# Performance work log

Measured on AMD Instinct MI355X. Metric: run time of the kernel, lower is better.

## Reference

```python
import jax, jax.numpy as jnp
import numpy as np

B, L, D, H, NL, DFF = 32, 64, 256, 8, 2, 2048
S, I, DSEM, DDENSE, DSPARSE = 16, 16, 128, 128, 128


def layer_norm(x, g, b, eps=1e-5):
    m = x.mean(-1, keepdims=True)
    v = ((x - m) ** 2).mean(-1, keepdims=True)
    return (x - m) / jnp.sqrt(v + eps) * g + b


def encoder_layer(x, ipw, ipb, ow, ob, g1, b1, g2, b2, f1w, f1b, f2w, f2b):
    # PyTorch TransformerEncoderLayer (post-norm, ReLU FFN, dropout inactive).
    b, t, d = x.shape
    dh = d // H
    qkv = x @ ipw.T + ipb  # (b,t,3d)
    q, k, v = jnp.split(qkv, 3, axis=-1)
    split_heads = lambda z: z.reshape(b, t, H, dh).transpose(0, 2, 1, 3)
    q, k, v = split_heads(q), split_heads(k), split_heads(v)
    att = jax.nn.softmax(jnp.einsum('bhqd,bhkd->bhqk', q, k) / np.float32(np.sqrt(dh)), axis=-1)
    o = jnp.einsum('bhqk,bhkd->bhqd', att, v).transpose(0, 2, 1, 3).reshape(b, t, d)
    x = layer_norm(x + o @ ow.T + ob, g1, b1)
    h = jax.nn.relu(x @ f1w.T + f1b) @ f2w.T + f2b
    return layer_norm(x + h, g2, b2)


def setup_inputs() -> dict:
    key = jax.random.key(0)
    ks = jax.random.split(key, 16)
    sc = np.float32(0.02)
    return dict(
        dense=jax.random.normal(ks[0], (B, L, DDENSE), jnp.float32),
        sparse=jax.random.normal(ks[1], (B, L, DSPARSE), jnp.float32),
        W_feat=jax.random.normal(ks[2], (DDENSE + DSPARSE, D), jnp.float32) * sc,
        b_feat=jnp.zeros((D,), jnp.float32),
        in_proj_w=jax.random.normal(ks[3], (NL, 3 * D, D), jnp.float32) * sc,
        in_proj_b=jnp.zeros((NL, 3 * D), jnp.float32),
        out_w=jax.random.normal(ks[4], (NL, D, D), jnp.float32) * sc,
        out_b=jnp.zeros((NL, D), jnp.float32),
        ln1_g=jnp.ones((NL, D), jnp.float32), ln1_b=jnp.zeros((NL, D), jnp.float32),
        ln2_g=jnp.ones((NL, D), jnp.float32), ln2_b=jnp.zeros((NL, D), jnp.float32),
        ff1_w=jax.random.normal(ks[5], (NL, DFF, D), jnp.float32) * sc,
        ff1_b=jnp.zeros((NL, DFF), jnp.float32),
        ff2_w=jax.random.normal(ks[6], (NL, D, DFF), jnp.float32) * sc,
        ff2_b=jnp.zeros((NL, D), jnp.float32),
        w_act=jax.random.normal(ks[7], (D, 1), jnp.float32) * sc,
        w_route_ws=jax.random.normal(ks[8], (L, S, D), jnp.float32) * sc,
        w_pose_ws=jax.random.normal(ks[9], (L, S, D, D), jnp.float32) * sc,
        w_route_si=jax.random.normal(ks[10], (S, I, D), jnp.float32) * sc,
        w_pose_si=jax.random.normal(ks[11], (S, I, D, D), jnp.float32) * sc,
        cls_w=jax.random.normal(ks[12], (DSEM, 2 * D), jnp.float32) * sc,
        cls_b=jnp.zeros((DSEM,), jnp.float32),
        inorm_g=jnp.ones((DSEM,), jnp.float32),
        inorm_b=jnp.zeros((DSEM,), jnp.float32),
    )


def reference(dense, sparse, W_feat, b_feat, in_proj_w, in_proj_b, out_w, out_b,
              ln1_g, ln1_b, ln2_g, ln2_b, ff1_w, ff1_b, ff2_w, ff2_b,
              w_act, w_route_ws, w_pose_ws, w_route_si, w_pose_si,
              cls_w, cls_b, inorm_g, inorm_b):
    # TokenFeaturizer: concat(dense, sparse) -> Linear -> (b,L,d)
    tok = jnp.concatenate([dense, sparse], axis=-1) @ W_feat + b_feat
    cls = tok.sum(axis=1, keepdims=True)  # einsum 'bld->bd' CLS token
    x = jnp.concatenate([tok, cls], axis=1)  # (b, L+1, d)
    for i in range(in_proj_w.shape[0]):
        x = encoder_layer(x, in_proj_w[i], in_proj_b[i], out_w[i], out_b[i],
                          ln1_g[i], ln1_b[i], ln2_g[i], ln2_b[i],
                          ff1_w[i], ff1_b[i], ff2_w[i], ff2_b[i])
    words, cls_tok = x[:, :L], x[:, L]  # (b,L,d), (b,d)

    # --- route words -> slots ('weighted_sig') ---
    a_words = jax.nn.sigmoid((words @ w_act)[..., 0])  # (b,L)
    c_ws = jax.nn.softmax(jnp.einsum('lsd,bld->bls', w_route_ws, words), axis=-1)
    a_num = jnp.einsum('bls,bl->bs', c_ws, a_words)
    a_slots = a_num / a_words.sum(axis=1, keepdims=True)
    u_hat = jnp.einsum('lsij,blj->blsi', w_pose_ws, words)  # (b,L,S,d)
    u_num = jnp.einsum('bls,bl,blsi->bsi', c_ws, a_words, u_hat)
    u_slots = u_num / a_num[..., None]  # (b,S,d)

    # --- route slots -> intents ---
    c_si = jax.nn.softmax(jnp.einsum('sid,bsd->bsi', w_route_si, u_slots), axis=-1)
    an = jnp.einsum('bsi,bs->bi', c_si, a_slots)
    a_intents = an / (a_slots.sum(axis=1, keepdims=True) + 1e-8)
    u_hat_i = jnp.einsum('sijk,bsk->bsik', w_pose_si, u_slots)  # (b,S,I,d)
    un = jnp.einsum('bsi,bs,bsik->bik', c_si, a_slots, u_hat_i)
    u_intents = un / (an[..., None] + 1e-8)  # (b,I,d)

    # argmax over intents, gather winning pose
    idx = jnp.argmax(a_intents, axis=-1)  # (b,)
    poses = u_intents[jnp.arange(u_intents.shape[0]), idx]  # (b,d)
    intents = jnp.concatenate([cls_tok, poses], axis=-1) @ cls_w.T + cls_b
    intents = layer_norm(intents, inorm_g, inorm_b)
    return (c_ws, intents)
```

## Files before the change

kernel.cpp:

```cpp
#include <hip/hip_runtime.h>
#include <hip/hip_bf16.h>
#include <math.h>

#define B_ 32
#define L_ 64
#define D_ 256
#define H_ 8
#define T_ 65
#define NT_ (B_*T_)
#define DFF_ 2048
#define S_ 16
#define I_ 16
#define DSEM_ 128

typedef __attribute__((ext_vector_type(8))) short bf16x8;
typedef __attribute__((ext_vector_type(4))) float f32x4;

typedef __attribute__((address_space(1))) const void gbl_void;
typedef __attribute__((address_space(3))) void lds_void;
#define GLOAD16(g, l) __builtin_amdgcn_global_load_lds((gbl_void*)(g), (lds_void*)(l), 16, 0, 0)

__device__ inline unsigned short f2bu(float f) {
  union { float f; unsigned u; } a; a.f = f;
  unsigned r = a.u + 0x7FFF + ((a.u >> 16) & 1);
  return (unsigned short)(r >> 16);
}
__device__ inline float b2f(unsigned short u) {
  union { unsigned u; float f; } a; a.u = ((unsigned)u) << 16;
  return a.f;
}

__device__ inline float wave_reduce_sum(float v) {
#pragma unroll
  for (int m = 32; m >= 1; m >>= 1) v += __shfl_xor(v, m, 64);
  return v;
}

__device__ inline float block_reduce_sum_256(float v, float* sred) {
  v = wave_reduce_sum(v);
  int tid = threadIdx.x;
  if ((tid & 63) == 0) sred[tid >> 6] = v;
  __syncthreads();
  float r = sred[0] + sred[1] + sred[2] + sred[3];
  __syncthreads();
  return r;
}

__global__ void concat_bf_kernel(const float* __restrict__ dense, const float* __restrict__ sparse,
                                 unsigned short* __restrict__ cat) {
  int idx = blockIdx.x * 256 + threadIdx.x;
  int r = idx >> 8, c = idx & 255;
  float v = (c < 128) ? dense[r * 128 + c] : sparse[r * 128 + (c - 128)];
  cat[idx] = f2bu(v);
}

__global__ void f2b4_kernel(const float* __restrict__ in, unsigned short* __restrict__ out, int n4) {
  int i = blockIdx.x * 256 + threadIdx.x;
  if (i < n4) {
    float4 v = ((const float4*)in)[i];
    short4 o;
    o.x = (short)f2bu(v.x); o.y = (short)f2bu(v.y);
    o.z = (short)f2bu(v.z); o.w = (short)f2bu(v.w);
    ((short4*)out)[i] = o;
  }
}

__global__ void transpose_f2b_kernel(const float* __restrict__ in, unsigned short* __restrict__ out) {
  int n = blockIdx.x, k = threadIdx.x;
  out[n * 256 + k] = f2bu(in[k * 256 + n]);
}

template <int ACT, int OUT_BF16, int NFRAG>
__global__ __launch_bounds__(256) void gemm_bf2_kernel(const unsigned short* __restrict__ A,
                                                       const unsigned short* __restrict__ W,
                                                       const float* __restrict__ bias,
                                                       float* __restrict__ Cf, unsigned short* __restrict__ Cb,
                                                       int M, int N, int K) {
  __shared__ __align__(16) unsigned short As[2][32 * 64];
  __shared__ __align__(16) unsigned short Bs[2][NFRAG * 64 * 64];
  int tid = threadIdx.x, wid = tid >> 6, lane = tid & 63;
  int row0 = blockIdx.y * 32, col0 = blockIdx.x * (64 * NFRAG);
  int lr = lane >> 3;
  int sc = ((lane & 7) ^ (lr & 7)) << 3;
  const unsigned short* Asrc = A + (size_t)(row0 + wid * 8 + lr) * K + sc;
  const unsigned short* Bsrc[2 * NFRAG];
#pragma unroll
  for (int p = 0; p < 2 * NFRAG; ++p)
    Bsrc[p] = W + (size_t)(col0 + wid * 16 * NFRAG + p * 8 + lr) * K + sc;
  unsigned short* AsW = &As[0][0] + wid * (8 * 64);
  unsigned short* BsW = &Bs[0][0] + wid * (16 * NFRAG * 64);

  f32x4 acc[2][NFRAG];
#pragma unroll
  for (int i = 0; i < 2; ++i)
#pragma unroll
    for (int j = 0; j < NFRAG; ++j) acc[i][j] = (f32x4){0.f, 0.f, 0.f, 0.f};

  GLOAD16(Asrc, AsW);
#pragma unroll
  for (int p = 0; p < 2 * NFRAG; ++p) GLOAD16(Bsrc[p], BsW + p * (8 * 64));

  int nk = K >> 6, cur = 0;
  int kg = lane >> 4, l15 = lane & 15;
  for (int kt = 0; kt < nk; ++kt) {
    __syncthreads();
    if (kt + 1 < nk) {
      int k0 = (kt + 1) << 6;
      GLOAD16(Asrc + k0, AsW + (cur ^ 1) * (32 * 64));
#pragma unroll
      for (int p = 0; p < 2 * NFRAG; ++p)
        GLOAD16(Bsrc[p] + k0, BsW + (cur ^ 1) * (NFRAG * 64 * 64) + p * (8 * 64));
    }
    const unsigned short* Ab = &As[cur][0];
    const unsigned short* Bb = &Bs[cur][0];
#pragma unroll
    for (int kk = 0; kk < 2; ++kk) {
      int cc = kk * 4 + kg;
      bf16x8 bfr[NFRAG];
#pragma unroll
      for (int fn = 0; fn < NFRAG; ++fn) {
        int rn = wid * 16 * NFRAG + fn * 16 + l15;
        bfr[fn] = *(const bf16x8*)&Bb[rn * 64 + ((cc ^ (rn & 7)) << 3)];
      }
#pragma unroll
      for (int fm = 0; fm < 2; ++fm) {
        int rm = fm * 16 + l15;
        bf16x8 afr = *(const bf16x8*)&Ab[rm * 64 + ((cc ^ (rm & 7)) << 3)];
#pragma unroll
        for (int fn = 0; fn < NFRAG; ++fn)
          acc[fm][fn] = __builtin_amdgcn_mfma_f32_16x16x32_bf16(afr, bfr[fn], acc[fm][fn], 0, 0, 0);
      }
    }
    cur ^= 1;
  }
#pragma unroll
  for (int fm = 0; fm < 2; ++fm) {
#pragma unroll
    for (int fn = 0; fn < NFRAG; ++fn) {
      int col = col0 + wid * 16 * NFRAG + fn * 16 + l15;
      float bi = bias[col];
      int rbase = row0 + fm * 16 + ((lane >> 4) << 2);
#pragma unroll
      for (int r = 0; r < 4; ++r) {
        int grow = rbase + r;
        float v = acc[fm][fn][r] + bi;
        if (ACT == 1) v = fmaxf(v, 0.f);
        if (OUT_BF16) Cb[(size_t)grow * N + col] = f2bu(v);
        else          Cf[(size_t)grow * N + col] = v;
      }
    }
  }
}

__global__ void build_x_kernel(const float* __restrict__ tok, float* __restrict__ x,
                               unsigned short* __restrict__ xbf) {
  int b = blockIdx.x, d = threadIdx.x;
  float s = 0.f;
  for (int l = 0; l < L_; ++l) {
    float v = tok[((size_t)(b * L_ + l)) * D_ + d];
    size_t o = ((size_t)(b * T_ + l)) * D_ + d;
    x[o] = v; xbf[o] = f2bu(v);
    s += v;
  }
  size_t o = ((size_t)(b * T_ + L_)) * D_ + d;
  x[o] = s; xbf[o] = f2bu(s);
}

__global__ __launch_bounds__(256) void attn_kernel(const unsigned short* __restrict__ qkv,
                                                   unsigned short* __restrict__ attn_out) {
  int bh = blockIdx.x;
  int b = bh >> 3, h = bh & 7;
  __shared__ float Q[T_][32], K[T_][32], V[T_][32];
  __shared__ float Sc[T_][T_ + 1];
  int tid = threadIdx.x;
  for (int idx = tid; idx < T_ * 32; idx += 256) {
    int t = idx >> 5, d = idx & 31;
    const unsigned short* base = qkv + ((size_t)(b * T_ + t)) * 768 + h * 32 + d;
    Q[t][d] = b2f(base[0]);
    K[t][d] = b2f(base[256]);
    V[t][d] = b2f(base[512]);
  }
  __syncthreads();
  for (int idx = tid; idx < T_ * T_; idx += 256) {
    int qi = idx / T_, ki = idx % T_;
    float s = 0.f;
#pragma unroll
    for (int d = 0; d < 32; ++d) s += Q[qi][d] * K[ki][d];
    Sc[qi][ki] = s * 0.17677669529663687f;
  }
  __syncthreads();
  if (tid < T_) {
    float mx = -1e30f;
    for (int k = 0; k < T_; ++k) mx = fmaxf(mx, Sc[tid][k]);
    float sum = 0.f;
    for (int k = 0; k < T_; ++k) { float e = expf(Sc[tid][k] - mx); Sc[tid][k] = e; sum += e; }
    float inv = 1.f / sum;
    for (int k = 0; k < T_; ++k) Sc[tid][k] *= inv;
  }
  __syncthreads();
  for (int idx = tid; idx < T_ * 32; idx += 256) {
    int t = idx >> 5, d = idx & 31;
    float acc = 0.f;
    for (int k = 0; k < T_; ++k) acc += Sc[t][k] * V[k][d];
    attn_out[((size_t)(b * T_ + t)) * D_ + h * 32 + d] = f2bu(acc);
  }
}

__global__ __launch_bounds__(256) void ln_residual_kernel(float* __restrict__ x, unsigned short* __restrict__ xbf,
                                                          const float* __restrict__ proj,
                                                          const float* __restrict__ g, const float* __restrict__ bb) {
  __shared__ float sred[4];
  int r = blockIdx.x, d = threadIdx.x;
  float v = x[(size_t)r * D_ + d] + proj[(size_t)r * D_ + d];
  float mean = block_reduce_sum_256(v, sred) * (1.f / 256.f);
  float dv = v - mean;
  float var = block_reduce_sum_256(dv * dv, sred) * (1.f / 256.f);
  float o = dv * (1.f / sqrtf(var + 1e-5f)) * g[d] + bb[d];
  x[(size_t)r * D_ + d] = o;
  xbf[(size_t)r * D_ + d] = f2bu(o);
}

__global__ __launch_bounds__(256) void cws_kernel(const float* __restrict__ x, const float* __restrict__ w_route,
                                                  const float* __restrict__ w_act, float* __restrict__ c_ws_out,
                                                  float* __restrict__ a_words) {
  int bl = blockIdx.x;
  int b = bl >> 6, l = bl & 63;
  __shared__ float word[256];
  __shared__ float logits[16];
  __shared__ float sred[4];
  int t = threadIdx.x;
  word[t] = x[((size_t)(b * T_ + l)) * D_ + t];
  __syncthreads();
  float pa = word[t] * w_act[t];
  float asum = block_reduce_sum_256(pa, sred);
  if (t == 0) a_words[b * 64 + l] = 1.f / (1.f + expf(-asum));
  int s = t >> 4, j0 = t & 15;
  float p = 0.f;
  for (int j = j0; j < 256; j += 16) p += w_route[((size_t)(l * 16 + s)) * 256 + j] * word[j];
#pragma unroll
  for (int m = 8; m >= 1; m >>= 1) p += __shfl_xor(p, m, 64);
  if (j0 == 0) logits[s] = p;
  __syncthreads();
  if (t < 16) {
    float mx = -1e30f;
#pragma unroll
    for (int k = 0; k < 16; ++k) mx = fmaxf(mx, logits[k]);
    float sum = 0.f;
#pragma unroll
    for (int k = 0; k < 16; ++k) sum += expf(logits[k] - mx);
    c_ws_out[(size_t)bl * 16 + t] = expf(logits[t] - mx) / sum;
  }
}

__global__ __launch_bounds__(64) void slot_agg_kernel(const float* __restrict__ c_ws, const float* __restrict__ a_words,
                                                      float* __restrict__ a_num, float* __restrict__ a_slots,
                                                      float* __restrict__ asl_sum) {
  int b = blockIdx.x, lane = threadIdx.x;
  float aw = a_words[b * 64 + lane];
  float asum = wave_reduce_sum(aw);
  float inv = 1.f / asum;
  float ssum = 0.f;
  for (int s = 0; s < 16; ++s) {
    float p = c_ws[((size_t)(b * 64 + lane)) * 16 + s] * aw;
    float r = wave_reduce_sum(p);
    if (lane == 0) {
      a_num[b * 16 + s] = r;
      a_slots[b * 16 + s] = r * inv;
      ssum += r * inv;
    }
  }
  if (lane == 0) asl_sum[b] = ssum;
}

__global__ __launch_bounds__(256, 4) void pose_ws2_kernel(const unsigned short* __restrict__ xbf,
                                                          const float* __restrict__ P,
                                                          const float* __restrict__ c_ws,
                                                          const float* __restrict__ a_words,
                                                          float* __restrict__ partial) {
  int lg = blockIdx.x >> 4, s = blockIdx.x & 15;
  __shared__ __align__(16) unsigned short Bs[32 * 256];
  int tid = threadIdx.x, wid = tid >> 6, lane = tid & 63;
  int kg = lane >> 4;
  f32x4 acc[4][2];
#pragma unroll
  for (int i = 0; i < 4; ++i)
#pragma unroll
    for (int j = 0; j < 2; ++j) acc[i][j] = (f32x4){0.f, 0.f, 0.f, 0.f};

#pragma unroll
  for (int li = 0; li < 2; ++li) {
    int l = lg + li * 32;
    __syncthreads();
    {
      int b = tid >> 3, c0 = (tid & 7) * 4;
      float w = c_ws[((size_t)(b * 64 + l)) * 16 + s] * a_words[b * 64 + l];
      const unsigned short* src = xbf + ((size_t)(b * T_ + l)) * D_;
#pragma unroll
      for (int j = 0; j < 4; ++j) {
        int c = c0 + j;
        union { float4 f4; unsigned short u[8]; } in, out;
        in.f4 = *(const float4*)(src + c * 8);
#pragma unroll
        for (int e = 0; e < 8; ++e) out.u[e] = f2bu(w * b2f(in.u[e]));
        *(float4*)&Bs[b * 256 + ((c ^ (b & 7)) << 3)] = out.f4;
      }
    }
    __syncthreads();
    const float* Pbase = P + (((size_t)(l * 16 + s)) << 16);
#pragma unroll
    for (int k0 = 0; k0 < 256; k0 += 64) {
#pragma unroll
      for (int kk = 0; kk < 2; ++kk) {
        int cc = (k0 >> 3) + kk * 4 + kg;
        bf16x8 bfr[2];
#pragma unroll
        for (int fn = 0; fn < 2; ++fn) {
          int rb = fn * 16 + (lane & 15);
          bfr[fn] = *(const bf16x8*)&Bs[rb * 256 + ((cc ^ (rb & 7)) << 3)];
        }
        int kbase = k0 + kk * 32 + kg * 8;
#pragma unroll
        for (int fm = 0; fm < 4; ++fm) {
          int row = wid * 64 + fm * 16 + (lane & 15);
          const float* src = Pbase + (size_t)row * 256 + kbase;
          float4 v0 = *(const float4*)src;
          float4 v1 = *(const float4*)(src + 4);
          union { bf16x8 b8; unsigned short u[8]; } pk;
          pk.u[0] = f2bu(v0.x); pk.u[1] = f2bu(v0.y); pk.u[2] = f2bu(v0.z); pk.u[3] = f2bu(v0.w);
          pk.u[4] = f2bu(v1.x); pk.u[5] = f2bu(v1.y); pk.u[6] = f2bu(v1.z); pk.u[7] = f2bu(v1.w);
          acc[fm][0] = __builtin_amdgcn_mfma_f32_16x16x32_bf16(pk.b8, bfr[0], acc[fm][0], 0, 0, 0);
          acc[fm][1] = __builtin_amdgcn_mfma_f32_16x16x32_bf16(pk.b8, bfr[1], acc[fm][1], 0, 0, 0);
        }
      }
    }
  }
  float* pout = partial + ((size_t)(lg * 16 + s)) * 8192;
#pragma unroll
  for (int fm = 0; fm < 4; ++fm) {
#pragma unroll
    for (int fn = 0; fn < 2; ++fn) {
      int b = fn * 16 + (lane & 15);
      int i0 = wid * 64 + fm * 16 + ((lane >> 4) << 2);
#pragma unroll
      for (int r = 0; r < 4; ++r)
        pout[(i0 + r) * 32 + b] = acc[fm][fn][r];
    }
  }
}

__global__ __launch_bounds__(256) void reduce_uslots_kernel(const float* __restrict__ partial,
                                                            const float* __restrict__ a_num,
                                                            float* __restrict__ u_slots) {
  int s = blockIdx.x >> 5, ic = blockIdx.x & 31;
  int t = threadIdx.x;
  int i = ic * 8 + (t >> 5), b = t & 31;
  size_t off = (size_t)s * 8192 + i * 32 + b;
  float a0 = 0.f, a1 = 0.f, a2 = 0.f, a3 = 0.f;
#pragma unroll
  for (int lg = 0; lg < 32; lg += 4) {
    a0 += partial[((size_t)(lg + 0) * 16) * 8192 + off];
    a1 += partial[((size_t)(lg + 1) * 16) * 8192 + off];
    a2 += partial[((size_t)(lg + 2) * 16) * 8192 + off];
    a3 += partial[((size_t)(lg + 3) * 16) * 8192 + off];
  }
  u_slots[((size_t)(b * 16 + s)) * 256 + i] = (a0 + a1 + a2 + a3) / a_num[b * 16 + s];
}

__global__ __launch_bounds__(256) void csi_kernel(const float* __restrict__ u_slots, const float* __restrict__ w_route_si,
                                                  float* __restrict__ c_si) {
  int bs = blockIdx.x;
  int s = bs & 15;
  __shared__ float row[256];
  __shared__ float logits[16];
  int t = threadIdx.x;
  row[t] = u_slots[(size_t)bs * 256 + t];
  __syncthreads();
  int i = t >> 4, j0 = t & 15;
  float p = 0.f;
  for (int j = j0; j < 256; j += 16) p += w_route_si[((size_t)(s * 16 + i)) * 256 + j] * row[j];
#pragma unroll
  for (int m = 8; m >= 1; m >>= 1) p += __shfl_xor(p, m, 64);
  if (j0 == 0) logits[i] = p;
  __syncthreads();
  if (t < 16) {
    float mx = -1e30f;
#pragma unroll
    for (int k = 0; k < 16; ++k) mx = fmaxf(mx, logits[k]);
    float sum = 0.f;
#pragma unroll
    for (int k = 0; k < 16; ++k) sum += expf(logits[k] - mx);
    c_si[(size_t)bs * 16 + t] = expf(logits[t] - mx) / sum;
  }
}

__global__ __launch_bounds__(64) void intent_agg_kernel(const float* __restrict__ c_si, const float* __restrict__ a_slots,
                                                        const float* __restrict__ asl_sum, float* __restrict__ an,
                                                        int* __restrict__ idxb) {
  int b = blockIdx.x, lane = threadIdx.x;
  __shared__ float an_s[16];
  if (lane < 16) {
    float acc = 0.f;
    for (int s = 0; s < 16; ++s) acc += c_si[((size_t)(b * 16 + s)) * 16 + lane] * a_slots[b * 16 + s];
    an[b * 16 + lane] = acc;
    an_s[lane] = acc;
  }
  __syncthreads();
  if (lane == 0) {
    float inv = 1.f / (asl_sum[b] + 1e-8f);
    int best = 0;
    float bv = an_s[0] * inv;
    for (int k = 1; k < 16; ++k) {
      float v = an_s[k] * inv;
      if (v > bv) { bv = v; best = k; }
    }
    idxb[b] = best;
  }
}

__global__ void pose_si_partial_kernel(const float* __restrict__ P, float* __restrict__ R4) {
  int si = blockIdx.x >> 2, jc = blockIdx.x & 3;
  int k = threadIdx.x;
  const float* base = P + (size_t)si * 65536 + (size_t)jc * 64 * 256 + k;
  float a0 = 0.f, a1 = 0.f, a2 = 0.f, a3 = 0.f;
#pragma unroll
  for (int j = 0; j < 64; j += 4) {
    a0 += base[(j + 0) * 256];
    a1 += base[(j + 1) * 256];
    a2 += base[(j + 2) * 256];
    a3 += base[(j + 3) * 256];
  }
  R4[(size_t)jc * 65536 + si * 256 + k] = a0 + a1 + a2 + a3;
}

__global__ void r4sum_kernel(const float* __restrict__ R4, float* __restrict__ R) {
  int idx = blockIdx.x * 256 + threadIdx.x;
  R[idx] = R4[idx] + R4[65536 + idx] + R4[131072 + idx] + R4[196608 + idx];
}

__global__ void un_kernel(const float* __restrict__ c_si, const float* __restrict__ a_slots,
                          const float* __restrict__ R, const float* __restrict__ u_slots,
                          const float* __restrict__ an, float* __restrict__ u_int) {
  int b = blockIdx.x >> 4, i = blockIdx.x & 15, k = threadIdx.x;
  float acc = 0.f;
  for (int s = 0; s < 16; ++s) {
    float w = c_si[((size_t)(b * 16 + s)) * 16 + i] * a_slots[b * 16 + s];
    acc += w * R[((size_t)(s * 16 + i)) * 256 + k] * u_slots[((size_t)(b * 16 + s)) * 256 + k];
  }
  u_int[((size_t)(b * 16 + i)) * 256 + k] = acc / (an[b * 16 + i] + 1e-8f);
}

__global__ __launch_bounds__(128) void final_kernel(const float* __restrict__ x, const float* __restrict__ u_int,
                                                    const int* __restrict__ idxb, const float* __restrict__ cls_w,
                                                    const float* __restrict__ cls_b, const float* __restrict__ g,
                                                    const float* __restrict__ bb, float* __restrict__ out) {
  int b = blockIdx.x, m = threadIdx.x;
  __shared__ float row[512];
  __shared__ float sred[2];
  int id = idxb[b];
  for (int d = m; d < 256; d += 128) {
    row[d] = x[((size_t)(b * T_ + L_)) * D_ + d];
    row[256 + d] = u_int[((size_t)(b * 16 + id)) * 256 + d];
  }
  __syncthreads();
  float acc = cls_b[m];
  for (int j = 0; j < 512; ++j) acc += cls_w[(size_t)m * 512 + j] * row[j];
  float v = wave_reduce_sum(acc);
  if ((m & 63) == 0) sred[m >> 6] = v;
  __syncthreads();
  float mean = (sred[0] + sred[1]) * (1.f / 128.f);
  __syncthreads();
  float dv = acc - mean;
  float v2 = wave_reduce_sum(dv * dv);
  if ((m & 63) == 0) sred[m >> 6] = v2;
  __syncthreads();
  float var = (sred[0] + sred[1]) * (1.f / 128.f);
  out[(size_t)b * 128 + m] = dv * (1.f / sqrtf(var + 1e-5f)) * g[m] + bb[m];
}

extern "C" void kernel_launch(void* const* d_in, const int* in_sizes, int n_in,
                              void* d_out, int out_size, void* d_ws, size_t ws_size,
                              hipStream_t stream) {
  (void)in_sizes; (void)n_in; (void)out_size; (void)ws_size;
  const float* dense      = (const float*)d_in[0];
  const float* sparse     = (const float*)d_in[1];
  const float* W_feat     = (const float*)d_in[2];
  const float* b_feat     = (const float*)d_in[3];
  const float* in_proj_w  = (const float*)d_in[4];
  const float* in_proj_b  = (const float*)d_in[5];
  const float* out_w      = (const float*)d_in[6];
  const float* out_b      = (const float*)d_in[7];
  const float* ln1_g      = (const float*)d_in[8];
  const float* ln1_b      = (const float*)d_in[9];
  const float* ln2_g      = (const float*)d_in[10];
  const float* ln2_b      = (const float*)d_in[11];
  const float* ff1_w      = (const float*)d_in[12];
  const float* ff1_b      = (const float*)d_in[13];
  const float* ff2_w      = (const float*)d_in[14];
  const float* ff2_b      = (const float*)d_in[15];
  const float* w_act      = (const float*)d_in[16];
  const float* w_route_ws = (const float*)d_in[17];
  const float* w_pose_ws  = (const float*)d_in[18];
  const float* w_route_si = (const float*)d_in[19];
  const float* w_pose_si  = (const float*)d_in[20];
  const float* cls_w      = (const float*)d_in[21];
  const float* cls_b      = (const float*)d_in[22];
  const float* inorm_g    = (const float*)d_in[23];
  const float* inorm_b    = (const float*)d_in[24];

  float* ws = (float*)d_ws;
  float* X       = ws;
  float* PROJ    = X + 532480;
  float* a_words = PROJ + 532480;
  float* a_num   = a_words + 2048;
  float* a_slots = a_num + 512;
  float* asl_sum = a_slots + 512;
  float* u_slots = asl_sum + 32;
  float* c_si    = u_slots + 131072;
  float* an      = c_si + 8192;
  float* Rbuf    = an + 512;
  float* u_int   = Rbuf + 65536;
  float* R4      = u_int + 131072;
  int*   idxb    = (int*)(R4 + 262144);

  unsigned short* bfb   = (unsigned short*)(R4 + 262144 + 32);
  unsigned short* Xbf   = bfb;
  unsigned short* QKVbf = Xbf + 532480;
  unsigned short* HAR   = QKVbf + 1597440;
  unsigned short* CATbf = HAR;
  unsigned short* ATTNbf= HAR + 2097152;
  unsigned short* wfeatT= HAR + 4259840;
  unsigned short* ipwB  = wfeatT + 65536;
  unsigned short* owB   = ipwB + 393216;
  unsigned short* f1wB  = owB + 131072;
  unsigned short* f2wB  = f1wB + 1048576;
  float* partial = (float*)QKVbf;

  float* c_ws_out    = (float*)d_out;
  float* intents_out = (float*)d_out + 32768;

  concat_bf_kernel<<<2048, 256, 0, stream>>>(dense, sparse, CATbf);
  transpose_f2b_kernel<<<256, 256, 0, stream>>>(W_feat, wfeatT);
  f2b4_kernel<<<384, 256, 0, stream>>>(in_proj_w, ipwB, 98304);
  f2b4_kernel<<<128, 256, 0, stream>>>(out_w, owB, 32768);
  f2b4_kernel<<<1024, 256, 0, stream>>>(ff1_w, f1wB, 262144);
  f2b4_kernel<<<1024, 256, 0, stream>>>(ff2_w, f2wB, 262144);

  gemm_bf2_kernel<0, 0, 1><<<dim3(4, 64), 256, 0, stream>>>(CATbf, wfeatT, b_feat, PROJ, nullptr, 2048, 256, 256);
  build_x_kernel<<<32, 256, 0, stream>>>(PROJ, X, Xbf);

  for (int layer = 0; layer < 2; ++layer) {
    const unsigned short* ipw = ipwB + (size_t)layer * 196608;
    const unsigned short* ow  = owB + (size_t)layer * 65536;
    const unsigned short* f1w = f1wB + (size_t)layer * 524288;
    const unsigned short* f2w = f2wB + (size_t)layer * 524288;
    const float* ipb = in_proj_b + (size_t)layer * 768;
    const float* ob  = out_b + (size_t)layer * 256;
    const float* g1  = ln1_g + (size_t)layer * 256;
    const float* b1  = ln1_b + (size_t)layer * 256;
    const float* g2  = ln2_g + (size_t)layer * 256;
    const float* b2  = ln2_b + (size_t)layer * 256;
    const float* f1b = ff1_b + (size_t)layer * DFF_;
    const float* f2b = ff2_b + (size_t)layer * 256;

    gemm_bf2_kernel<0, 1, 2><<<dim3(6, 65), 256, 0, stream>>>(Xbf, ipw, ipb, nullptr, QKVbf, NT_, 768, 256);
    attn_kernel<<<B_ * H_, 256, 0, stream>>>(QKVbf, ATTNbf);
    gemm_bf2_kernel<0, 0, 1><<<dim3(4, 65), 256, 0, stream>>>(ATTNbf, ow, ob, PROJ, nullptr, NT_, 256, 256);
    ln_residual_kernel<<<NT_, 256, 0, stream>>>(X, Xbf, PROJ, g1, b1);
    gemm_bf2_kernel<1, 1, 2><<<dim3(16, 65), 256, 0, stream>>>(Xbf, f1w, f1b, nullptr, HAR, NT_, DFF_, 256);
    gemm_bf2_kernel<0, 0, 1><<<dim3(4, 65), 256, 0, stream>>>(HAR, f2w, f2b, PROJ, nullptr, NT_, 256, DFF_);
    ln_residual_kernel<<<NT_, 256, 0, stream>>>(X, Xbf, PROJ, g2, b2);
  }

  cws_kernel<<<2048, 256, 0, stream>>>(X, w_route_ws, w_act, c_ws_out, a_words);
  slot_agg_kernel<<<32, 64, 0, stream>>>(c_ws_out, a_words, a_num, a_slots, asl_sum);
  pose_ws2_kernel<<<512, 256, 0, stream>>>(Xbf, w_pose_ws, c_ws_out, a_words, partial);
  reduce_uslots_kernel<<<512, 256, 0, stream>>>(partial, a_num, u_slots);
  pose_si_partial_kernel<<<1024, 256, 0, stream>>>(w_pose_si, R4);
  r4sum_kernel<<<256, 256, 0, stream>>>(R4, Rbuf);
  csi_kernel<<<512, 256, 0, stream>>>(u_slots, w_route_si, c_si);
  intent_agg_kernel<<<32, 64, 0, stream>>>(c_si, a_slots, asl_sum, an, idxb);
  un_kernel<<<512, 256, 0, stream>>>(c_si, a_slots, Rbuf, u_slots, an, u_int);
  final_kernel<<<32, 128, 0, stream>>>(X, u_int, idxb, cls_w, cls_b, inorm_g, inorm_b, intents_out);
}
```

Measured before the change: 291.2 us.

## Fuse out-proj/FFN2 GEMMs with LayerNorm, merge weight conversions, compute only winning intent

Out-projection and FFN2 GEMMs are replaced by a GEMM that covers the full 256-wide row per block and applies bias, residual and LayerNorm in its epilogue, removing the separate LN kernels and the PROJ round trip. Weight bf16 conversions are merged into one launch, and the W_feat transpose now goes through an LDS tile so reads and writes are coalesced. Softmax in attention is spread across 4 threads per row, and the intent pose is computed only for the argmax intent. The tradeoff is that the fused GEMM launches only 65 blocks, so the K=2048 FFN2 GEMM may be under-parallelised. LN variance now comes from E[x^2]-mean^2, which is less numerically stable.

```diff
diff --git a/kernel.cpp b/kernel.cpp
--- a/kernel.cpp
+++ b/kernel.cpp
@@ -54,20 +54,40 @@
   cat[idx] = f2bu(v);
 }
 
-__global__ void f2b4_kernel(const float* __restrict__ in, unsigned short* __restrict__ out, int n4) {
+__global__ void conv_all_kernel(const float* __restrict__ ipw, const float* __restrict__ ow,
+                                const float* __restrict__ f1w, const float* __restrict__ f2w,
+                                unsigned short* __restrict__ ipwB, unsigned short* __restrict__ owB,
+                                unsigned short* __restrict__ f1wB, unsigned short* __restrict__ f2wB) {
   int i = blockIdx.x * 256 + threadIdx.x;
-  if (i < n4) {
-    float4 v = ((const float4*)in)[i];
-    short4 o;
-    o.x = (short)f2bu(v.x); o.y = (short)f2bu(v.y);
-    o.z = (short)f2bu(v.z); o.w = (short)f2bu(v.w);
-    ((short4*)out)[i] = o;
-  }
-}
-
-__global__ void transpose_f2b_kernel(const float* __restrict__ in, unsigned short* __restrict__ out) {
-  int n = blockIdx.x, k = threadIdx.x;
-  out[n * 256 + k] = f2bu(in[k * 256 + n]);
+  const float* src; unsigned short* dst; int off;
+  if (i < 98304)       { src = ipw; dst = ipwB; off = i; }
+  else if (i < 131072) { src = ow;  dst = owB;  off = i - 98304; }
+  else if (i < 393216) { src = f1w; dst = f1wB; off = i - 131072; }
+  else                 { src = f2w; dst = f2wB; off = i - 393216; }
+  float4 v = ((const float4*)src)[off];
+  short4 o;
+  o.x = (short)f2bu(v.x); o.y = (short)f2bu(v.y);
+  o.z = (short)f2bu(v.z); o.w = (short)f2bu(v.w);
+  ((short4*)dst)[off] = o;
+}
+
+__global__ __launch_bounds__(256) void transpose_f2b_kernel(const float* __restrict__ in,
+                                                            unsigned short* __restrict__ out) {
+  __shared__ float t[64][65];
+  int blk = blockIdx.x;
+  int k0 = (blk & 3) * 64, n0 = (blk >> 2) * 64;
+  int wid = threadIdx.x >> 6, lane = threadIdx.x & 63;
+#pragma unroll
+  for (int p = 0; p < 16; ++p) {
+    int kk = p * 4 + wid;
+    t[kk][lane] = in[(size_t)(k0 + kk) * 256 + n0 + lane];
+  }
+  __syncthreads();
+#pragma unroll
+  for (int p = 0; p < 16; ++p) {
+    int nn = p * 4 + wid;
+    out[(size_t)(n0 + nn) * 256 + k0 + lane] = f2bu(t[lane][nn]);
+  }
 }
 
 template <int ACT, int OUT_BF16, int NFRAG>
@@ -152,6 +172,136 @@
   }
 }
 
+__global__ __launch_bounds__(256) void gemm_ln_kernel(const unsigned short* __restrict__ A,
+                                                      const unsigned short* __restrict__ W,
+                                                      const float* __restrict__ bias,
+                                                      const float* __restrict__ gw, const float* __restrict__ gb,
+                                                      float* X, unsigned short* __restrict__ xbf,
+                                                      int K) {
+  __shared__ __align__(16) unsigned short As[2][32 * 64];
+  __shared__ __align__(16) unsigned short Bs[2][4 * 64 * 64];
+  __shared__ float sred[4][32], sredq[4][32];
+  int tid = threadIdx.x, wid = tid >> 6, lane = tid & 63;
+  int row0 = blockIdx.y * 32;
+  int lr = lane >> 3;
+  int sc = ((lane & 7) ^ (lr & 7)) << 3;
+  const unsigned short* Asrc = A + (size_t)(row0 + wid * 8 + lr) * K + sc;
+  const unsigned short* Bsrc[8];
+#pragma unroll
+  for (int p = 0; p < 8; ++p)
+    Bsrc[p] = W + (size_t)(wid * 64 + p * 8 + lr) * K + sc;
+  unsigned short* AsW = &As[0][0] + wid * (8 * 64);
+  unsigned short* BsW = &Bs[0][0] + wid * (64 * 64);
+
+  f32x4 acc[2][4];
+#pragma unroll
+  for (int i = 0; i < 2; ++i)
+#pragma unroll
+    for (int j = 0; j < 4; ++j) acc[i][j] = (f32x4){0.f, 0.f, 0.f, 0.f};
+
+  GLOAD16(Asrc, AsW);
+#pragma unroll
+  for (int p = 0; p < 8; ++p) GLOAD16(Bsrc[p], BsW + p * (8 * 64));
+
+  int nk = K >> 6, cur = 0;
+  int kg = lane >> 4, l15 = lane & 15;
+  for (int kt = 0; kt < nk; ++kt) {
+    __syncthreads();
+    if (kt + 1 < nk) {
+      int k0 = (kt + 1) << 6;
+      GLOAD16(Asrc + k0, AsW + (cur ^ 1) * (32 * 64));
+#pragma unroll
+      for (int p = 0; p < 8; ++p)
+        GLOAD16(Bsrc[p] + k0, BsW + (cur ^ 1) * (4 * 64 * 64) + p * (8 * 64));
+    }
+    const unsigned short* Ab = &As[cur][0];
+    const unsigned short* Bb = &Bs[cur][0];
+#pragma unroll
+    for (int kk = 0; kk < 2; ++kk) {
+      int cc = kk * 4 + kg;
+      bf16x8 bfr[4];
+#pragma unroll
+      for (int fn = 0; fn < 4; ++fn) {
+        int rn = wid * 64 + fn * 16 + l15;
+        bfr[fn] = *(const bf16x8*)&Bb[rn * 64 + ((cc ^ (rn & 7)) << 3)];
+      }
+#pragma unroll
+      for (int fm = 0; fm < 2; ++fm) {
+        int rm = fm * 16 + l15;
+        bf16x8 afr = *(const bf16x8*)&Ab[rm * 64 + ((cc ^ (rm & 7)) << 3)];
+#pragma unroll
+        for (int fn = 0; fn < 4; ++fn)
+          acc[fm][fn] = __builtin_amdgcn_mfma_f32_16x16x32_bf16(afr, bfr[fn], acc[fm][fn], 0, 0, 0);
+      }
+    }
+    cur ^= 1;
+  }
+  int g = lane >> 4;
+  float v[2][4][4];
+  float rs[2][4], rq[2][4];
+#pragma unroll
+  for (int fm = 0; fm < 2; ++fm)
+#pragma unroll
+    for (int r = 0; r < 4; ++r) { rs[fm][r] = 0.f; rq[fm][r] = 0.f; }
+#pragma unroll
+  for (int fm = 0; fm < 2; ++fm) {
+    int grow0 = row0 + fm * 16 + g * 4;
+#pragma unroll
+    for (int fn = 0; fn < 4; ++fn) {
+      int col = wid * 64 + fn * 16 + l15;
+      float bi = bias[col];
+#pragma unroll
+      for (int r = 0; r < 4; ++r) {
+        float val = acc[fm][fn][r] + bi + X[(size_t)(grow0 + r) * 256 + col];
+        v[fm][fn][r] = val;
+        rs[fm][r] += val;
+        rq[fm][r] += val * val;
+      }
+    }
+  }
+#pragma unroll
+  for (int m = 1; m <= 8; m <<= 1) {
+#pragma unroll
+    for (int fm = 0; fm < 2; ++fm)
+#pragma unroll
+      for (int r = 0; r < 4; ++r) {
+        rs[fm][r] += __shfl_xor(rs[fm][r], m, 64);
+        rq[fm][r] += __shfl_xor(rq[fm][r], m, 64);
+      }
+  }
+  if (l15 == 0) {
+#pragma unroll
+    for (int fm = 0; fm < 2; ++fm)
+#pragma unroll
+      for (int r = 0; r < 4; ++r) {
+        int row = fm * 16 + g * 4 + r;
+        sred[wid][row] = rs[fm][r];
+        sredq[wid][row] = rq[fm][r];
+      }
+  }
+  __syncthreads();
+#pragma unroll
+  for (int fm = 0; fm < 2; ++fm) {
+#pragma unroll
+    for (int r = 0; r < 4; ++r) {
+      int row = fm * 16 + g * 4 + r;
+      float tsum = sred[0][row] + sred[1][row] + sred[2][row] + sred[3][row];
+      float tsq = sredq[0][row] + sredq[1][row] + sredq[2][row] + sredq[3][row];
+      float mean = tsum * (1.f / 256.f);
+      float var = tsq * (1.f / 256.f) - mean * mean;
+      float rstd = 1.f / sqrtf(var + 1e-5f);
+      int grow = row0 + row;
+#pragma unroll
+      for (int fn = 0; fn < 4; ++fn) {
+        int col = wid * 64 + fn * 16 + l15;
+        float o = (v[fm][fn][r] - mean) * rstd * gw[col] + gb[col];
+        X[(size_t)grow * 256 + col] = o;
+        xbf[(size_t)grow * 256 + col] = f2bu(o);
+      }
+    }
+  }
+}
+
 __global__ void build_x_kernel(const float* __restrict__ tok, float* __restrict__ x,
                                unsigned short* __restrict__ xbf) {
   int b = blockIdx.x, d = threadIdx.x;
@@ -189,13 +339,20 @@
     Sc[qi][ki] = s * 0.17677669529663687f;
   }
   __syncthreads();
-  if (tid < T_) {
-    float mx = -1e30f;
-    for (int k = 0; k < T_; ++k) mx = fmaxf(mx, Sc[tid][k]);
-    float sum = 0.f;
-    for (int k = 0; k < T_; ++k) { float e = expf(Sc[tid][k] - mx); Sc[tid][k] = e; sum += e; }
-    float inv = 1.f / sum;
-    for (int k = 0; k < T_; ++k) Sc[tid][k] *= inv;
+  {
+    int q = tid & 3;
+    for (int row = tid >> 2; row < T_; row += 64) {
+      float mx = -1e30f;
+      for (int k = q; k < T_; k += 4) mx = fmaxf(mx, Sc[row][k]);
+      mx = fmaxf(mx, __shfl_xor(mx, 1, 64));
+      mx = fmaxf(mx, __shfl_xor(mx, 2, 64));
+      float sum = 0.f;
+      for (int k = q; k < T_; k += 4) { float e = expf(Sc[row][k] - mx); Sc[row][k] = e; sum += e; }
+      sum += __shfl_xor(sum, 1, 64);
+      sum += __shfl_xor(sum, 2, 64);
+      float inv = 1.f / sum;
+      for (int k = q; k < T_; k += 4) Sc[row][k] *= inv;
+    }
   }
   __syncthreads();
   for (int idx = tid; idx < T_ * 32; idx += 256) {
@@ -204,20 +361,6 @@
     for (int k = 0; k < T_; ++k) acc += Sc[t][k] * V[k][d];
     attn_out[((size_t)(b * T_ + t)) * D_ + h * 32 + d] = f2bu(acc);
   }
-}
-
-__global__ __launch_bounds__(256) void ln_residual_kernel(float* __restrict__ x, unsigned short* __restrict__ xbf,
-                                                          const float* __restrict__ proj,
-                                                          const float* __restrict__ g, const float* __restrict__ bb) {
-  __shared__ float sred[4];
-  int r = blockIdx.x, d = threadIdx.x;
-  float v = x[(size_t)r * D_ + d] + proj[(size_t)r * D_ + d];
-  float mean = block_reduce_sum_256(v, sred) * (1.f / 256.f);
-  float dv = v - mean;
-  float var = block_reduce_sum_256(dv * dv, sred) * (1.f / 256.f);
-  float o = dv * (1.f / sqrtf(var + 1e-5f)) * g[d] + bb[d];
-  x[(size_t)r * D_ + d] = o;
-  xbf[(size_t)r * D_ + d] = f2bu(o);
 }
 
 __global__ __launch_bounds__(256) void cws_kernel(const float* __restrict__ x, const float* __restrict__ w_route,
@@ -437,29 +580,30 @@
   R[idx] = R4[idx] + R4[65536 + idx] + R4[131072 + idx] + R4[196608 + idx];
 }
 
-__global__ void un_kernel(const float* __restrict__ c_si, const float* __restrict__ a_slots,
-                          const float* __restrict__ R, const float* __restrict__ u_slots,
-                          const float* __restrict__ an, float* __restrict__ u_int) {
-  int b = blockIdx.x >> 4, i = blockIdx.x & 15, k = threadIdx.x;
+__global__ void un32_kernel(const float* __restrict__ c_si, const float* __restrict__ a_slots,
+                            const float* __restrict__ R, const float* __restrict__ u_slots,
+                            const float* __restrict__ an, const int* __restrict__ idxb,
+                            float* __restrict__ u_pose) {
+  int b = blockIdx.x, k = threadIdx.x;
+  int i = idxb[b];
   float acc = 0.f;
   for (int s = 0; s < 16; ++s) {
     float w = c_si[((size_t)(b * 16 + s)) * 16 + i] * a_slots[b * 16 + s];
     acc += w * R[((size_t)(s * 16 + i)) * 256 + k] * u_slots[((size_t)(b * 16 + s)) * 256 + k];
   }
-  u_int[((size_t)(b * 16 + i)) * 256 + k] = acc / (an[b * 16 + i] + 1e-8f);
-}
-
-__global__ __launch_bounds__(128) void final_kernel(const float* __restrict__ x, const float* __restrict__ u_int,
-                                                    const int* __restrict__ idxb, const float* __restrict__ cls_w,
+  u_pose[(size_t)b * 256 + k] = acc / (an[b * 16 + i] + 1e-8f);
+}
+
+__global__ __launch_bounds__(128) void final_kernel(const float* __restrict__ x, const float* __restrict__ u_pose,
+                                                    const float* __restrict__ cls_w,
                                                     const float* __restrict__ cls_b, const float* __restrict__ g,
                                                     const float* __restrict__ bb, float* __restrict__ out) {
   int b = blockIdx.x, m = threadIdx.x;
   __shared__ float row[512];
   __shared__ float sred[2];
-  int id = idxb[b];
   for (int d = m; d < 256; d += 128) {
     row[d] = x[((size_t)(b * T_ + L_)) * D_ + d];
-    row[256 + d] = u_int[((size_t)(b * 16 + id)) * 256 + d];
+    row[256 + d] = u_pose[(size_t)b * 256 + d];
   }
   __syncthreads();
   float acc = cls_b[m];
@@ -518,8 +662,8 @@
   float* c_si    = u_slots + 131072;
   float* an      = c_si + 8192;
   float* Rbuf    = an + 512;
-  float* u_int   = Rbuf + 65536;
-  float* R4      = u_int + 131072;
+  float* u_pose  = Rbuf + 65536;
+  float* R4      = u_pose + 8192;
   int*   idxb    = (int*)(R4 + 262144);
 
   unsigned short* bfb   = (unsigned short*)(R4 + 262144 + 32);
@@ -539,11 +683,8 @@
   float* intents_out = (float*)d_out + 32768;
 
   concat_bf_kernel<<<2048, 256, 0, stream>>>(dense, sparse, CATbf);
-  transpose_f2b_kernel<<<256, 256, 0, stream>>>(W_feat, wfeatT);
-  f2b4_kernel<<<384, 256, 0, stream>>>(in_proj_w, ipwB, 98304);
-  f2b4_kernel<<<128, 256, 0, stream>>>(out_w, owB, 32768);
-  f2b4_kernel<<<1024, 256, 0, stream>>>(ff1_w, f1wB, 262144);
-  f2b4_kernel<<<1024, 256, 0, stream>>>(ff2_w, f2wB, 262144);
+  transpose_f2b_kernel<<<16, 256, 0, stream>>>(W_feat, wfeatT);
+  conv_all_kernel<<<2560, 256, 0, stream>>>(in_proj_w, out_w, ff1_w, ff2_w, ipwB, owB, f1wB, f2wB);
 
   gemm_bf2_kernel<0, 0, 1><<<dim3(4, 64), 256, 0, stream>>>(CATbf, wfeatT, b_feat, PROJ, nullptr, 2048, 256, 256);
   build_x_kernel<<<32, 256, 0, stream>>>(PROJ, X, Xbf);
@@ -564,11 +705,9 @@
 
     gemm_bf2_kernel<0, 1, 2><<<dim3(6, 65), 256, 0, stream>>>(Xbf, ipw, ipb, nullptr, QKVbf, NT_, 768, 256);
     attn_kernel<<<B_ * H_, 256, 0, stream>>>(QKVbf, ATTNbf);
-    gemm_bf2_kernel<0, 0, 1><<<dim3(4, 65), 256, 0, stream>>>(ATTNbf, ow, ob, PROJ, nullptr, NT_, 256, 256);
-    ln_residual_kernel<<<NT_, 256, 0, stream>>>(X, Xbf, PROJ, g1, b1);
+    gemm_ln_kernel<<<dim3(1, 65), 256, 0, stream>>>(ATTNbf, ow, ob, g1, b1, X, Xbf, 256);
     gemm_bf2_kernel<1, 1, 2><<<dim3(16, 65), 256, 0, stream>>>(Xbf, f1w, f1b, nullptr, HAR, NT_, DFF_, 256);
-    gemm_bf2_kernel<0, 0, 1><<<dim3(4, 65), 256, 0, stream>>>(HAR, f2w, f2b, PROJ, nullptr, NT_, 256, DFF_);
-    ln_residual_kernel<<<NT_, 256, 0, stream>>>(X, Xbf, PROJ, g2, b2);
+    gemm_ln_kernel<<<dim3(1, 65), 256, 0, stream>>>(HAR, f2w, f2b, g2, b2, X, Xbf, 2048);
   }
 
   cws_kernel<<<2048, 256, 0, stream>>>(X, w_route_ws, w_act, c_ws_out, a_words);
@@ -579,6 +718,6 @@
   r4sum_kernel<<<256, 256, 0, stream>>>(R4, Rbuf);
   csi_kernel<<<512, 256, 0, stream>>>(u_slots, w_route_si, c_si);
   intent_agg_kernel<<<32, 64, 0, stream>>>(c_si, a_slots, asl_sum, an, idxb);
-  un_kernel<<<512, 256, 0, stream>>>(c_si, a_slots, Rbuf, u_slots, an, u_int);
-  final_kernel<<<32, 128, 0, stream>>>(X, u_int, idxb, cls_w, cls_b, inorm_g, inorm_b, intents_out);
-}
+  un32_kernel<<<32, 256, 0, stream>>>(c_si, a_slots, Rbuf, u_slots, an, idxb, u_pose);
+  final_kernel<<<32, 128, 0, stream>>>(X, u_pose, cls_w, cls_b, inorm_g, inorm_b, intents_out);
+}
```

Result: slower. 304.2 us (+4.5%).
